# Optimization experiments

Measured on AMD Instinct MI355X. Metric: run time of the kernel, lower is better.

Reference implementation:

```python
import jax, jax.numpy as jnp
import numpy as np

# mamba-130m dims (n_layers reduced to 4 for single-device tractability)
B, L, D, DI, N, R, K, V, NL = 2, 512, 768, 1536, 16, 48, 4, 50280, 4


def setup_inputs() -> dict:
    key = jax.random.key(0)
    ks = jax.random.split(key, 10)
    s = 0.02
    return {
        "question_ids": jax.random.randint(ks[0], (B, L), 0, V, dtype=jnp.int32),
        "question_mask": jnp.ones((B, L), dtype=jnp.int32),
        "answer_ids": jax.random.randint(ks[1], (B, L), 0, V, dtype=jnp.int32),
        "answer_mask": jnp.ones((B, L), dtype=jnp.int32),
        "embed": jax.random.normal(ks[2], (V, D), jnp.float32) * s,
        "in_proj_w": jax.random.normal(ks[3], (NL, D, 2 * DI), jnp.float32) * s,
        "conv_w": jax.random.normal(ks[4], (NL, DI, K), jnp.float32) * s,
        "conv_b": jnp.zeros((NL, DI), jnp.float32),
        "x_proj_w": jax.random.normal(ks[5], (NL, DI, R + 2 * N), jnp.float32) * s,
        "dt_proj_w": jax.random.normal(ks[6], (NL, R, DI), jnp.float32) * s,
        # bias ~ -4.6 so softplus(dt) ~ 0.01, like mamba's dt init range
        "dt_proj_b": jnp.full((NL, DI), -4.6, jnp.float32),
        "A_log": jnp.broadcast_to(jnp.log(jnp.arange(1, N + 1, dtype=jnp.float32)), (NL, DI, N)) + jnp.zeros((NL, DI, N), jnp.float32),
        "D_param": jnp.ones((NL, DI), jnp.float32),
        "out_proj_w": jax.random.normal(ks[7], (NL, DI, D), jnp.float32) * s,
        "norm_w": jnp.ones((NL, D), jnp.float32),
        "norm_f_w": jnp.ones((D,), jnp.float32),
    }


def _rms(x, w, eps=1e-5):
    return x * jax.lax.rsqrt(jnp.mean(x * x, axis=-1, keepdims=True) + eps) * w


def _selective_scan(dA, dBu, Ct):
    # dA, dBu: (B, L, DI, N); Ct: (B, L, N)
    def step(h, xs):
        a, b = xs
        h = a * h + b
        return h, h

    h0 = jnp.zeros((dA.shape[0], dA.shape[2], dA.shape[3]), dA.dtype)  # (B, DI, N)
    _, hs = jax.lax.scan(step, h0, (jnp.swapaxes(dA, 0, 1), jnp.swapaxes(dBu, 0, 1)))
    hs = jnp.swapaxes(hs, 0, 1)  # (B, L, DI, N)
    return jnp.einsum('bldn,bln->bld', hs, Ct)


def _block(x, p):
    ipw, cw, cb, xpw, dtw, dtb, Alog, Dp, opw, nw = p
    h = _rms(x, nw)
    xz = h @ ipw                      # (B, L, 2*DI)
    u, z = xz[..., :DI], xz[..., DI:]
    # depthwise causal conv, kernel K
    up = jnp.pad(u, ((0, 0), (K - 1, 0), (0, 0)))
    uc = sum(up[:, k:k + u.shape[1], :] * cw[:, k] for k in range(K)) + cb
    uc = jax.nn.silu(uc)
    proj = uc @ xpw                   # (B, L, R+2N)
    dt = jax.nn.softplus(proj[..., :R] @ dtw + dtb)
    Bt = proj[..., R:R + N]
    Ct = proj[..., R + N:]
    A = -jnp.exp(Alog)                # (DI, N)
    dA = jnp.exp(dt[..., None] * A)   # (B, L, DI, N)
    dBu = (dt * uc)[..., None] * Bt[:, :, None, :]
    y = _selective_scan(dA, dBu, Ct) + uc * Dp
    y = y * jax.nn.silu(z)
    return x + y @ opw


def _lm_loss(ids, mask, embed, layers, norm_f_w):
    x = embed[ids] * mask[..., None].astype(embed.dtype)
    for p in layers:
        x = _block(x, p)
    x = _rms(x, norm_f_w)
    logits = x @ embed.T              # tied lm head, (B, L, V)
    logp = jax.nn.log_softmax(logits[:, :-1], axis=-1)
    lbl = ids[:, 1:]
    nll = -jnp.take_along_axis(logp, lbl[..., None], axis=-1)[..., 0]
    m = mask[:, 1:].astype(logp.dtype)
    return jnp.sum(nll * m) / jnp.maximum(jnp.sum(m), 1.0)


def reference(question_ids, question_mask, answer_ids, answer_mask, embed, in_proj_w, conv_w, conv_b, x_proj_w, dt_proj_w, dt_proj_b, A_log, D_param, out_proj_w, norm_w, norm_f_w):
    layers = [
        (in_proj_w[l], conv_w[l], conv_b[l], x_proj_w[l], dt_proj_w[l], dt_proj_b[l], A_log[l], D_param[l], out_proj_w[l], norm_w[l])
        for l in range(NL)
    ]
    loss_q = _lm_loss(question_ids, question_mask, embed, layers, norm_f_w)
    loss_a = _lm_loss(answer_ids, answer_mask, embed, layers, norm_f_w)
    return loss_a + loss_q
```

## Files before the change

### kernel.cpp

```cpp
#include <hip/hip_runtime.h>
#include <hip/hip_bf16.h>
#include <cstdint>
#include <cstddef>

#define T_TOK   2048
#define DM      768
#define DI      1536
#define NST     16
#define RRANK   48
#define KCONV   4
#define VOCAB   50280
#define NLAYER  4
#define SEQL    512
#define NTILE_V 197
#define NCHUNK  8
#define CHL     64
#define NCAT    1568

typedef __bf16 bf16x8 __attribute__((ext_vector_type(8)));
typedef float  f32x4  __attribute__((ext_vector_type(4)));

__device__ inline unsigned short f2b(float f) {
  union { float f; unsigned u; } v; v.f = f;
  unsigned r = v.u + 0x7FFFu + ((v.u >> 16) & 1u);
  return (unsigned short)(r >> 16);
}
__device__ inline float b2f(unsigned short h) {
  union { unsigned u; float f; } v; v.u = ((unsigned)h) << 16;
  return v.f;
}

__device__ inline void gload_lds16(const unsigned short* g, unsigned short* l) {
  __builtin_amdgcn_global_load_lds(
      (const __attribute__((address_space(1))) void*)g,
      (__attribute__((address_space(3))) void*)l, 16, 0, 0);
}

__global__ __launch_bounds__(256) void transpose_conv_kernel(
    const float* __restrict__ src, unsigned short* __restrict__ dst,
    int R, int C, int Rpad) {
  __shared__ float tile[32][33];
  const float* s = src + (size_t)blockIdx.z * R * C;
  unsigned short* d = dst + (size_t)blockIdx.z * C * Rpad;
  int c0 = blockIdx.x * 32, r0 = blockIdx.y * 32;
  int tx = threadIdx.x & 31, ty = threadIdx.x >> 5;
  #pragma unroll
  for (int i = 0; i < 32; i += 8) {
    int r = r0 + ty + i, c = c0 + tx;
    tile[ty + i][tx] = (r < R && c < C) ? s[(size_t)r * C + c] : 0.f;
  }
  __syncthreads();
  #pragma unroll
  for (int i = 0; i < 32; i += 8) {
    int c = c0 + ty + i, r = r0 + tx;
    if (c < C && r < Rpad) d[(size_t)c * Rpad + r] = f2b(tile[tx][ty + i]);
  }
}

__global__ __launch_bounds__(256) void cvt_embed_kernel(
    const float* __restrict__ e, unsigned short* __restrict__ eb) {
  const int n4 = VOCAB * DM / 4;
  for (int i = blockIdx.x * 256 + threadIdx.x; i < n4; i += gridDim.x * 256) {
    float4 f = *(const float4*)(e + (size_t)i * 4);
    union { unsigned long long u; unsigned short h[4]; } pk;
    pk.h[0] = f2b(f.x); pk.h[1] = f2b(f.y); pk.h[2] = f2b(f.z); pk.h[3] = f2b(f.w);
    *(unsigned long long*)(eb + (size_t)i * 4) = pk.u;
  }
}

__global__ __launch_bounds__(256) void wcat_bc_kernel(
    const float* __restrict__ xpw, unsigned short* __restrict__ wcat) {
  int l = blockIdx.y;
  int idx = blockIdx.x * 256 + threadIdx.x;
  int n = idx / DI, k = idx - n * DI;
  wcat[(size_t)l * NCAT * DI + (size_t)n * DI + k] =
      f2b(xpw[(size_t)l * DI * 80 + (size_t)k * 80 + 48 + n]);
}

__global__ __launch_bounds__(256) void wdt_kernel(
    const float* __restrict__ xpw, const float* __restrict__ dtw,
    unsigned short* __restrict__ wcat) {
  __shared__ float xs[64][49];
  __shared__ float ds[48][64];
  int l = blockIdx.z;
  int k0 = blockIdx.x * 64, n0 = blockIdx.y * 64;
  const float* xp = xpw + (size_t)l * DI * 80;
  const float* dp = dtw + (size_t)l * RRANK * DI;
  int tid = threadIdx.x;
  {
    int row = tid >> 2, cg = (tid & 3) * 12;
    #pragma unroll
    for (int c = 0; c < 12; ++c)
      xs[row][cg + c] = xp[(size_t)(k0 + row) * 80 + cg + c];
    int col = tid & 63, rb = tid >> 6;
    #pragma unroll
    for (int i = 0; i < 12; ++i)
      ds[rb + 4 * i][col] = dp[(size_t)(rb + 4 * i) * DI + n0 + col];
  }
  __syncthreads();
  int tx = tid & 63, ty = tid >> 6;
  float acc[16] = {};
  #pragma unroll 8
  for (int r = 0; r < 48; ++r) {
    float xv = xs[tx][r];
    #pragma unroll
    for (int i = 0; i < 16; ++i) acc[i] += xv * ds[r][ty + 4 * i];
  }
  unsigned short* wl = wcat + (size_t)l * NCAT * DI + (size_t)(32 + n0) * DI;
  #pragma unroll
  for (int i = 0; i < 16; ++i)
    wl[(size_t)(ty + 4 * i) * DI + k0 + tx] = f2b(acc[i]);
}

__global__ __launch_bounds__(256) void gather_rms_kernel(
    const int* __restrict__ qids, const int* __restrict__ qmask,
    const int* __restrict__ aids, const int* __restrict__ amask,
    const float* __restrict__ embed, const float* __restrict__ w,
    float* __restrict__ x, unsigned short* __restrict__ h) {
  int t = blockIdx.x;
  int seq = t >> 9, pos = t & 511;
  const int* ids = (seq < 2) ? qids : aids;
  const int* msk = (seq < 2) ? qmask : amask;
  int s2 = seq & 1;
  int id = ids[s2 * SEQL + pos];
  float m = (float)msk[s2 * SEQL + pos];
  const float* er = embed + (size_t)id * DM;
  float v[3], ss = 0.f;
  #pragma unroll
  for (int j = 0; j < 3; ++j) {
    int d = threadIdx.x + j * 256;
    float vv = er[d] * m;
    x[(size_t)t * DM + d] = vv;
    v[j] = vv; ss += vv * vv;
  }
  for (int o = 1; o < 64; o <<= 1) ss += __shfl_xor(ss, o);
  __shared__ float wsum[4];
  if ((threadIdx.x & 63) == 0) wsum[threadIdx.x >> 6] = ss;
  __syncthreads();
  ss = wsum[0] + wsum[1] + wsum[2] + wsum[3];
  float sc = rsqrtf(ss / (float)DM + 1e-5f);
  #pragma unroll
  for (int j = 0; j < 3; ++j) {
    int d = threadIdx.x + j * 256;
    h[(size_t)t * DM + d] = f2b(v[j] * sc * w[d]);
  }
}

__global__ __launch_bounds__(256) void resid_rms_kernel(
    float* __restrict__ x, const float* __restrict__ part,
    const float* __restrict__ w, unsigned short* __restrict__ h) {
  int t = blockIdx.x;
  float v[3];
  float ss = 0.f;
  #pragma unroll
  for (int j = 0; j < 3; ++j) {
    int d = threadIdx.x + j * 256;
    size_t o = (size_t)t * DM + d;
    float xv = x[o] + part[o] + part[(size_t)T_TOK * DM + o] +
               part[(size_t)2 * T_TOK * DM + o] + part[(size_t)3 * T_TOK * DM + o];
    x[o] = xv; v[j] = xv; ss += xv * xv;
  }
  for (int o = 1; o < 64; o <<= 1) ss += __shfl_xor(ss, o);
  __shared__ float wsum[4];
  if ((threadIdx.x & 63) == 0) wsum[threadIdx.x >> 6] = ss;
  __syncthreads();
  ss = wsum[0] + wsum[1] + wsum[2] + wsum[3];
  float sc = rsqrtf(ss / (float)DM + 1e-5f);
  #pragma unroll
  for (int j = 0; j < 3; ++j) {
    int d = threadIdx.x + j * 256;
    h[(size_t)t * DM + d] = f2b(v[j] * sc * w[d]);
  }
}

template <int EPI>
__global__ __launch_bounds__(256) void gemm_bf16_kernel(
    const unsigned short* __restrict__ A, int lda,
    const unsigned short* __restrict__ B, int ldb,
    float* __restrict__ C, float* __restrict__ CT, int ldc,
    const float* __restrict__ bias,
    int M, int N, int K, int mtiles) {
  __shared__ __attribute__((aligned(16))) unsigned short As[128 * 64];
  __shared__ __attribute__((aligned(16))) unsigned short Bs[128 * 64];
  int bid = blockIdx.x;
  int m0 = (bid % mtiles) * 128;
  int rest = bid / mtiles;
  int n0, split = 0;
  int ntil = (N + 127) >> 7;
  if (EPI == 6) { split = rest / ntil; n0 = (rest % ntil) * 128; }
  else n0 = rest * 128;
  const unsigned short* Ap = (EPI == 6) ? A + (size_t)split * K : A;
  const unsigned short* Bp = (EPI == 6) ? B + (size_t)split * K : B;
  int tid = threadIdx.x;
  int lane = tid & 63, w = tid >> 6;
  int wr = w >> 1, wc = w & 1;
  f32x4 acc[4][4] = {};

  int lrow = lane >> 3;
  int lcol = (((lane & 7) ^ (lrow & 7)) & 7) * 8;
  auto STAGE = [&](int k0) {
    #pragma unroll
    for (int it = 0; it < 4; ++it) {
      int r = w * 32 + it * 8;
      gload_lds16(Ap + (size_t)(m0 + r + lrow) * lda + k0 + lcol, &As[r * 64]);
      int br = n0 + r + lrow; if (br > N - 1) br = N - 1;
      gload_lds16(Bp + (size_t)br * ldb + k0 + lcol, &Bs[r * 64]);
    }
  };

  int nst = K / 64;
  int rA = wr * 64 + (lane & 15);
  int rB = wc * 64 + (lane & 15);
  int sw = lane & 7, ckb = lane >> 4;
  for (int s = 0; s < nst; ++s) {
    STAGE(s * 64);
    __syncthreads();
    __builtin_amdgcn_s_setprio(1);
    #pragma unroll
    for (int ks = 0; ks < 2; ++ks) {
      int ca = (((ks * 4 + ckb) ^ sw) & 7) * 8;
      bf16x8 a[4], b[4];
      #pragma unroll
      for (int i = 0; i < 4; ++i) a[i] = *(const bf16x8*)(&As[(rA + i * 16) * 64 + ca]);
      #pragma unroll
      for (int i = 0; i < 4; ++i) b[i] = *(const bf16x8*)(&Bs[(rB + i * 16) * 64 + ca]);
      #pragma unroll
      for (int mi = 0; mi < 4; ++mi)
        #pragma unroll
        for (int ni = 0; ni < 4; ++ni)
          acc[mi][ni] = __builtin_amdgcn_mfma_f32_16x16x32_bf16(a[mi], b[ni], acc[mi][ni], 0, 0, 0);
    }
    __builtin_amdgcn_s_setprio(0);
    __syncthreads();
  }

  int g = lane >> 4, c = lane & 15;
  #pragma unroll
  for (int mi = 0; mi < 4; ++mi)
    #pragma unroll
    for (int ni = 0; ni < 4; ++ni) {
      int col = n0 + wc * 64 + ni * 16 + c;
      int row0 = m0 + wr * 64 + mi * 16 + g * 4;
      if (EPI == 6) {
        if (col < N) {
          #pragma unroll
          for (int r = 0; r < 4; ++r)
            C[((size_t)split * M + row0 + r) * ldc + col] = acc[mi][ni][r];
        }
      }
      if (EPI == 7) {
        if (col < DI) {
          #pragma unroll
          for (int r = 0; r < 4; ++r)
            C[(size_t)(row0 + r) * DI + col] = acc[mi][ni][r];
        } else {
          float4 o; float* ov = (float*)&o;
          #pragma unroll
          for (int r = 0; r < 4; ++r) {
            float zv = acc[mi][ni][r];
            ov[r] = zv / (1.f + __expf(-zv));
          }
          *(float4*)(&CT[(size_t)(col - DI) * T_TOK + row0]) = o;
        }
      }
      if (EPI == 8) {
        if (col < 32) {
          float4 o; float* ov = (float*)&o;
          #pragma unroll
          for (int r = 0; r < 4; ++r) ov[r] = acc[mi][ni][r];
          *(float4*)(&C[(size_t)col * T_TOK + row0]) = o;
        } else if (col < NCAT) {
          float4 o; float* ov = (float*)&o;
          #pragma unroll
          for (int r = 0; r < 4; ++r) {
            float xv = acc[mi][ni][r] + bias[col - 32];
            ov[r] = (xv > 20.f) ? xv : log1pf(__expf(xv));
          }
          *(float4*)(&CT[(size_t)(col - 32) * T_TOK + row0]) = o;
        }
      }
    }
}

__global__ __launch_bounds__(512) void gemm_lse_kernel(
    const unsigned short* __restrict__ A,
    const unsigned short* __restrict__ B,
    float* __restrict__ pmax, float* __restrict__ psum,
    int mtiles) {
  __shared__ __attribute__((aligned(16))) unsigned short As[128 * 64];
  __shared__ __attribute__((aligned(16))) unsigned short Bs[256 * 64];
  __shared__ float lmax[128][4];
  __shared__ float lsum[128][4];
  const int K = DM, Nv = VOCAB;
  int bid = blockIdx.x;
  int m0 = (bid % mtiles) * 128;
  int n0 = (bid / mtiles) * 256;
  int tid = threadIdx.x;
  int lane = tid & 63, w = tid >> 6;
  int wr = w >> 2, wc = w & 3;
  f32x4 acc[4][4] = {};

  int lrow = lane >> 3;
  int lcol = (((lane & 7) ^ (lrow & 7)) & 7) * 8;
  auto STAGE = [&](int k0) {
    #pragma unroll
    for (int it = 0; it < 2; ++it) {
      int r = w * 16 + it * 8;
      gload_lds16(A + (size_t)(m0 + r + lrow) * K + k0 + lcol, &As[r * 64]);
    }
    #pragma unroll
    for (int it = 0; it < 4; ++it) {
      int r = w * 32 + it * 8;
      int br = n0 + r + lrow; if (br > Nv - 1) br = Nv - 1;
      gload_lds16(B + (size_t)br * K + k0 + lcol, &Bs[r * 64]);
    }
  };

  const int nst = K / 64;
  int rA = wr * 64 + (lane & 15);
  int rB = wc * 64 + (lane & 15);
  int sw = lane & 7, ckb = lane >> 4;
  for (int s = 0; s < nst; ++s) {
    STAGE(s * 64);
    __syncthreads();
    __builtin_amdgcn_s_setprio(1);
    #pragma unroll
    for (int ks = 0; ks < 2; ++ks) {
      int ca = (((ks * 4 + ckb) ^ sw) & 7) * 8;
      bf16x8 a[4], b[4];
      #pragma unroll
      for (int i = 0; i < 4; ++i) a[i] = *(const bf16x8*)(&As[(rA + i * 16) * 64 + ca]);
      #pragma unroll
      for (int i = 0; i < 4; ++i) b[i] = *(const bf16x8*)(&Bs[(rB + i * 16) * 64 + ca]);
      #pragma unroll
      for (int mi = 0; mi < 4; ++mi)
        #pragma unroll
        for (int ni = 0; ni < 4; ++ni)
          acc[mi][ni] = __builtin_amdgcn_mfma_f32_16x16x32_bf16(a[mi], b[ni], acc[mi][ni], 0, 0, 0);
    }
    __builtin_amdgcn_s_setprio(0);
    __syncthreads();
  }

  int g = lane >> 4, c = lane & 15;
  #pragma unroll
  for (int mi = 0; mi < 4; ++mi) {
    #pragma unroll
    for (int r = 0; r < 4; ++r) {
      float mx = -INFINITY;
      #pragma unroll
      for (int ni = 0; ni < 4; ++ni) {
        int col = n0 + wc * 64 + ni * 16 + c;
        float v = (col < Nv) ? acc[mi][ni][r] : -INFINITY;
        mx = fmaxf(mx, v);
      }
      mx = fmaxf(mx, __shfl_xor(mx, 1, 16));
      mx = fmaxf(mx, __shfl_xor(mx, 2, 16));
      mx = fmaxf(mx, __shfl_xor(mx, 4, 16));
      mx = fmaxf(mx, __shfl_xor(mx, 8, 16));
      float ssum = 0.f;
      #pragma unroll
      for (int ni = 0; ni < 4; ++ni) {
        int col = n0 + wc * 64 + ni * 16 + c;
        if (col < Nv) ssum += __expf(acc[mi][ni][r] - mx);
      }
      ssum += __shfl_xor(ssum, 1, 16);
      ssum += __shfl_xor(ssum, 2, 16);
      ssum += __shfl_xor(ssum, 4, 16);
      ssum += __shfl_xor(ssum, 8, 16);
      if (c == 0) {
        int rl = wr * 64 + mi * 16 + g * 4 + r;
        lmax[rl][wc] = mx;
        lsum[rl][wc] = ssum;
      }
    }
  }
  __syncthreads();
  if (tid < 128) {
    float m0v = lmax[tid][0], m1 = lmax[tid][1], m2 = lmax[tid][2], m3 = lmax[tid][3];
    float Mx = fmaxf(fmaxf(m0v, m1), fmaxf(m2, m3));
    float S = lsum[tid][0] * __expf(m0v - Mx) + lsum[tid][1] * __expf(m1 - Mx) +
              lsum[tid][2] * __expf(m2 - Mx) + lsum[tid][3] * __expf(m3 - Mx);
    int row = m0 + tid;
    int nb = n0 >> 8;
    pmax[(size_t)row * NTILE_V + nb] = Mx;
    psum[(size_t)row * NTILE_V + nb] = S;
  }
}

__global__ __launch_bounds__(256) void conv_silu_kernel(
    const float* __restrict__ ur, const float* __restrict__ cw,
    const float* __restrict__ cb,
    unsigned short* __restrict__ ucbf, float* __restrict__ ucT) {
  __shared__ float xu[67][64];
  __shared__ float ou[64][65];
  int t0 = blockIdx.x * 64;
  int ch0 = blockIdx.y * 64;
  int tid = threadIdx.x;
  int cx = tid & 63, ty = tid >> 6;
  bool seq_start = (t0 & 511) == 0;
  for (int r = ty; r < 67; r += 4) {
    int tg = t0 - 3 + r;
    float v = 0.f;
    if (r >= 3 || !seq_start) v = ur[(size_t)tg * DI + ch0 + cx];
    xu[r][cx] = v;
  }
  __syncthreads();
  int ch = ch0 + cx;
  float4 wv = *(const float4*)(cw + ch * 4);
  float bias = cb[ch];
  #pragma unroll
  for (int i = 0; i < 16; ++i) {
    int tr = ty * 16 + i;
    float a = bias + xu[tr][cx] * wv.x + xu[tr + 1][cx] * wv.y +
              xu[tr + 2][cx] * wv.z + xu[tr + 3][cx] * wv.w;
    float s = a / (1.f + __expf(-a));
    ucbf[(size_t)(t0 + tr) * DI + ch] = f2b(s);
    ou[tr][cx] = s;
  }
  __syncthreads();
  int tx = tid & 63, cy = tid >> 6;
  #pragma unroll
  for (int i = 0; i < 16; ++i) {
    int chi = cy * 16 + i;
    ucT[(size_t)(ch0 + chi) * T_TOK + t0 + tx] = ou[tx][chi];
  }
}

__global__ __launch_bounds__(256) void scan_sum_kernel(
    const float* __restrict__ dtT, const float* __restrict__ ucT,
    const float* __restrict__ BCt, const float* __restrict__ Alog,
    float* __restrict__ Pbuf, float* __restrict__ Fbuf) {
  int bc = blockIdx.x / 96;
  int idx = (blockIdx.x % 96) * 256 + threadIdx.x;
  int n = idx & 15, d = idx >> 4;
  int b = bc >> 3, chunk = bc & 7;
  float A = -__expf(Alog[d * NST + n]);
  int t0 = b * SEQL + chunk * CHL;
  const float4* dp = (const float4*)(dtT + (size_t)d * T_TOK + t0);
  const float4* up = (const float4*)(ucT + (size_t)d * T_TOK + t0);
  const float4* Bp = (const float4*)(BCt + (size_t)n * T_TOK + t0);
  float h = 0.f, sdt = 0.f;
  #pragma unroll
  for (int q = 0; q < CHL / 4; ++q) {
    float4 d4 = dp[q], u4 = up[q], B4 = Bp[q];
    float a;
    a = __expf(d4.x * A); h = fmaf(a, h, d4.x * u4.x * B4.x);
    a = __expf(d4.y * A); h = fmaf(a, h, d4.y * u4.y * B4.y);
    a = __expf(d4.z * A); h = fmaf(a, h, d4.z * u4.z * B4.z);
    a = __expf(d4.w * A); h = fmaf(a, h, d4.w * u4.w * B4.w);
    sdt += d4.x + d4.y + d4.z + d4.w;
  }
  size_t s = ((size_t)bc * DI + d) * NST + n;
  Pbuf[s] = __expf(A * sdt);
  Fbuf[s] = h;
}

__global__ __launch_bounds__(256) void scan_emit_kernel(
    const float* __restrict__ dtT, const float* __restrict__ ucT,
    const float* __restrict__ BCt, const float* __restrict__ zsT,
    const float* __restrict__ Alog, const float* __restrict__ Dpar,
    const float* __restrict__ Pbuf, const float* __restrict__ Fbuf,
    unsigned short* __restrict__ yg) {
  int bc = blockIdx.x / 96;
  int idx = (blockIdx.x % 96) * 256 + threadIdx.x;
  int n = idx & 15, d = idx >> 4;
  int b = bc >> 3, chunk = bc & 7;
  float A = -__expf(Alog[d * NST + n]);
  float Dpv = Dpar[d];
  float h = 0.f;
  for (int j = 0; j < chunk; ++j) {
    size_t s = (((size_t)(b * NCHUNK + j)) * DI + d) * NST + n;
    h = Fbuf[s] + Pbuf[s] * h;
  }
  int t0 = b * SEQL + chunk * CHL;
  const float4* dp = (const float4*)(dtT + (size_t)d * T_TOK + t0);
  const float4* up = (const float4*)(ucT + (size_t)d * T_TOK + t0);
  const float4* Bp = (const float4*)(BCt + (size_t)n * T_TOK + t0);
  const float4* Cp = (const float4*)(BCt + (size_t)(NST + n) * T_TOK + t0);
  const float4* zp = (const float4*)(zsT + (size_t)d * T_TOK + t0);
  unsigned short* yp = yg + (size_t)t0 * DI + d;
  #pragma unroll 4
  for (int q = 0; q < CHL / 4; ++q) {
    float4 d4 = dp[q], u4 = up[q], B4 = Bp[q], C4 = Cp[q], z4 = zp[q];
    float y0, y1, y2, y3, a, cc;
    a = __expf(d4.x * A); h = fmaf(a, h, d4.x * u4.x * B4.x); cc = h * C4.x;
    cc += __shfl_xor(cc, 1, 16); cc += __shfl_xor(cc, 2, 16);
    cc += __shfl_xor(cc, 4, 16); cc += __shfl_xor(cc, 8, 16);
    y0 = (cc + u4.x * Dpv) * z4.x;
    a = __expf(d4.y * A); h = fmaf(a, h, d4.y * u4.y * B4.y); cc = h * C4.y;
    cc += __shfl_xor(cc, 1, 16); cc += __shfl_xor(cc, 2, 16);
    cc += __shfl_xor(cc, 4, 16); cc += __shfl_xor(cc, 8, 16);
    y1 = (cc + u4.y * Dpv) * z4.y;
    a = __expf(d4.z * A); h = fmaf(a, h, d4.z * u4.z * B4.z); cc = h * C4.z;
    cc += __shfl_xor(cc, 1, 16); cc += __shfl_xor(cc, 2, 16);
    cc += __shfl_xor(cc, 4, 16); cc += __shfl_xor(cc, 8, 16);
    y2 = (cc + u4.z * Dpv) * z4.z;
    a = __expf(d4.w * A); h = fmaf(a, h, d4.w * u4.w * B4.w); cc = h * C4.w;
    cc += __shfl_xor(cc, 1, 16); cc += __shfl_xor(cc, 2, 16);
    cc += __shfl_xor(cc, 4, 16); cc += __shfl_xor(cc, 8, 16);
    y3 = (cc + u4.w * Dpv) * z4.w;
    if (n == 0) {
      yp[(size_t)(q * 4 + 0) * DI] = f2b(y0);
      yp[(size_t)(q * 4 + 1) * DI] = f2b(y1);
      yp[(size_t)(q * 4 + 2) * DI] = f2b(y2);
      yp[(size_t)(q * 4 + 3) * DI] = f2b(y3);
    }
  }
}

__global__ __launch_bounds__(256) void lse_label_kernel(
    const float* __restrict__ pmax, const float* __restrict__ psum,
    const unsigned short* __restrict__ h, const unsigned short* __restrict__ eb,
    const int* __restrict__ qids, const int* __restrict__ qmask,
    const int* __restrict__ aids, const int* __restrict__ amask,
    float* __restrict__ nllm, float* __restrict__ mrow) {
  int row = blockIdx.x * 4 + (threadIdx.x >> 6);
  int lane = threadIdx.x & 63;
  const float* pm = pmax + (size_t)row * NTILE_V;
  const float* ps = psum + (size_t)row * NTILE_V;
  float m = -INFINITY;
  for (int j = lane; j < NTILE_V; j += 64) m = fmaxf(m, pm[j]);
  for (int o = 1; o < 64; o <<= 1) m = fmaxf(m, __shfl_xor(m, o));
  float s = 0.f;
  for (int j = lane; j < NTILE_V; j += 64) s += ps[j] * __expf(pm[j] - m);
  for (int o = 1; o < 64; o <<= 1) s += __shfl_xor(s, o);
  float lse = m + __logf(s);
  int pos = row & 511, seq = row >> 9;
  float nll = 0.f, mv = 0.f;
  if (pos != 511) {
    const int* ids = (seq < 2) ? qids : aids;
    const int* msk = (seq < 2) ? qmask : amask;
    int lbl = ids[(seq & 1) * SEQL + pos + 1];
    mv = (float)msk[(seq & 1) * SEQL + pos + 1];
    const unsigned short* hr = h + (size_t)row * DM;
    const unsigned short* er = eb + (size_t)lbl * DM;
    float dt = 0.f;
    for (int k = lane; k < DM; k += 64) dt += b2f(hr[k]) * b2f(er[k]);
    for (int o = 1; o < 64; o <<= 1) dt += __shfl_xor(dt, o);
    nll = (lse - dt) * mv;
  }
  if (lane == 0) { nllm[row] = nll; mrow[row] = mv; }
}

__global__ __launch_bounds__(256) void loss2_kernel(
    const float* __restrict__ nllm, const float* __restrict__ mrow,
    float* __restrict__ out) {
  float nq = 0.f, dq = 0.f, na = 0.f, da = 0.f;
  for (int row = threadIdx.x; row < T_TOK; row += 256) {
    int seq = row >> 9;
    if (seq < 2) { nq += nllm[row]; dq += mrow[row]; }
    else         { na += nllm[row]; da += mrow[row]; }
  }
  for (int o = 1; o < 64; o <<= 1) {
    nq += __shfl_xor(nq, o); dq += __shfl_xor(dq, o);
    na += __shfl_xor(na, o); da += __shfl_xor(da, o);
  }
  __shared__ float red[4][4];
  int w = threadIdx.x >> 6;
  if ((threadIdx.x & 63) == 0) { red[w][0] = nq; red[w][1] = dq; red[w][2] = na; red[w][3] = da; }
  __syncthreads();
  if (threadIdx.x == 0) {
    nq = 0.f; dq = 0.f; na = 0.f; da = 0.f;
    for (int i = 0; i < 4; ++i) { nq += red[i][0]; dq += red[i][1]; na += red[i][2]; da += red[i][3]; }
    float lq = nq / fmaxf(dq, 1.f);
    float la = na / fmaxf(da, 1.f);
    out[0] = lq + la;
  }
}

extern "C" void kernel_launch(void* const* d_in, const int* in_sizes, int n_in,
                              void* d_out, int out_size, void* d_ws, size_t ws_size,
                              hipStream_t stream) {
  const int*   qids  = (const int*)d_in[0];
  const int*   qmask = (const int*)d_in[1];
  const int*   aids  = (const int*)d_in[2];
  const int*   amask = (const int*)d_in[3];
  const float* embed = (const float*)d_in[4];
  const float* ipw   = (const float*)d_in[5];
  const float* cw    = (const float*)d_in[6];
  const float* cb    = (const float*)d_in[7];
  const float* xpw   = (const float*)d_in[8];
  const float* dtw   = (const float*)d_in[9];
  const float* dtb   = (const float*)d_in[10];
  const float* Alog  = (const float*)d_in[11];
  const float* Dp    = (const float*)d_in[12];
  const float* opw   = (const float*)d_in[13];
  const float* nw    = (const float*)d_in[14];
  const float* nfw   = (const float*)d_in[15];

  char* wp = (char*)d_ws;
  auto alloc = [&](size_t bytes) { char* p = wp; wp += (bytes + 255) & ~(size_t)255; return p; };

  float*          x      = (float*)alloc((size_t)T_TOK * DM * 4);
  unsigned short* hbf    = (unsigned short*)alloc((size_t)T_TOK * DM * 2);
  float*          ur     = (float*)alloc((size_t)T_TOK * DI * 4);
  unsigned short* ucbf   = (unsigned short*)alloc((size_t)T_TOK * DI * 2);
  unsigned short* ygbf   = (unsigned short*)alloc((size_t)T_TOK * DI * 2);
  float*          ucT    = (float*)alloc((size_t)DI * T_TOK * 4);
  float*          zsT    = (float*)alloc((size_t)DI * T_TOK * 4);
  float*          dtT    = (float*)alloc((size_t)DI * T_TOK * 4);
  float*          BCt    = (float*)alloc((size_t)2 * NST * T_TOK * 4);
  float*          Pbuf   = (float*)alloc((size_t)4 * NCHUNK * DI * NST * 4);
  float*          Fbuf   = (float*)alloc((size_t)4 * NCHUNK * DI * NST * 4);
  float*          opart  = (float*)alloc((size_t)4 * T_TOK * DM * 4);
  unsigned short* ipw_t  = (unsigned short*)alloc((size_t)NLAYER * 2 * DI * DM * 2);
  unsigned short* opw_t  = (unsigned short*)alloc((size_t)NLAYER * DM * DI * 2);
  unsigned short* wcat   = (unsigned short*)alloc((size_t)NLAYER * NCAT * DI * 2);
  unsigned short* embbf  = (unsigned short*)alloc((size_t)VOCAB * DM * 2);
  float*          pmax   = (float*)alloc((size_t)T_TOK * NTILE_V * 4);
  float*          psum   = (float*)alloc((size_t)T_TOK * NTILE_V * 4);
  float*          nllm   = (float*)alloc((size_t)T_TOK * 4);
  float*          mrow   = (float*)alloc((size_t)T_TOK * 4);

  transpose_conv_kernel<<<dim3(96, 24, NLAYER), 256, 0, stream>>>(ipw, ipw_t, DM, 2 * DI, DM);
  transpose_conv_kernel<<<dim3(24, 48, NLAYER), 256, 0, stream>>>(opw, opw_t, DI, DM, DI);
  cvt_embed_kernel<<<2048, 256, 0, stream>>>(embed, embbf);
  wcat_bc_kernel<<<dim3(192, NLAYER), 256, 0, stream>>>(xpw, wcat);
  wdt_kernel<<<dim3(24, 24, NLAYER), 256, 0, stream>>>(xpw, dtw, wcat);

  gather_rms_kernel<<<T_TOK, 256, 0, stream>>>(qids, qmask, aids, amask, embed, nw, x, hbf);

  const int mt = T_TOK / 128;
  for (int l = 0; l < NLAYER; ++l) {
    gemm_bf16_kernel<7><<<mt * (2 * DI / 128), 256, 0, stream>>>(
        hbf, DM, ipw_t + (size_t)l * 2 * DI * DM, DM, ur, zsT, DI,
        nullptr, T_TOK, 2 * DI, DM, mt);
    conv_silu_kernel<<<dim3(T_TOK / 64, DI / 64), 256, 0, stream>>>(
        ur, cw + (size_t)l * DI * KCONV, cb + (size_t)l * DI, ucbf, ucT);
    gemm_bf16_kernel<8><<<mt * 13, 256, 0, stream>>>(
        ucbf, DI, wcat + (size_t)l * NCAT * DI, DI, BCt, dtT, 0,
        dtb + (size_t)l * DI, T_TOK, NCAT, DI, mt);
    scan_sum_kernel<<<32 * 96, 256, 0, stream>>>(
        dtT, ucT, BCt, Alog + (size_t)l * DI * NST, Pbuf, Fbuf);
    scan_emit_kernel<<<32 * 96, 256, 0, stream>>>(
        dtT, ucT, BCt, zsT, Alog + (size_t)l * DI * NST, Dp + (size_t)l * DI,
        Pbuf, Fbuf, ygbf);
    gemm_bf16_kernel<6><<<mt * (DM / 128) * 4, 256, 0, stream>>>(
        ygbf, DI, opw_t + (size_t)l * DM * DI, DI, opart, nullptr, DM,
        nullptr, T_TOK, DM, DI / 4, mt);
    resid_rms_kernel<<<T_TOK, 256, 0, stream>>>(
        x, opart, (l < NLAYER - 1) ? (nw + (l + 1) * DM) : nfw, hbf);
  }

  gemm_lse_kernel<<<mt * NTILE_V, 512, 0, stream>>>(hbf, embbf, pmax, psum, mt);
  lse_label_kernel<<<T_TOK / 4, 256, 0, stream>>>(
      pmax, psum, hbf, embbf, qids, qmask, aids, amask, nllm, mrow);
  loss2_kernel<<<1, 256, 0, stream>>>(nllm, mrow, (float*)d_out);
}
```

Measured before the change: 1.181 ms.

## Unfold fused x_proj/dt_proj weight into low-rank two-GEMM chain

Previously the dt part of x_proj was pre-multiplied with dt_proj into a 1568-wide concatenated weight, making each layer's projection a full 2048x1568x1536 GEMM. Now x_proj runs as a narrow 80-column split-K GEMM, followed by a reduce kernel that writes the bf16 projection and the B/C rows. A separate K=64 GEMM with a softplus epilogue then produces dt. This exploits the rank-48 bottleneck to cut FLOPs sharply, at the cost of two extra launches and a partial-sum round trip per layer.

```diff
diff --git a/kernel.cpp b/kernel.cpp
--- a/kernel.cpp
+++ b/kernel.cpp
@@ -15,7 +15,6 @@
 #define NTILE_V 197
 #define NCHUNK  8
 #define CHL     64
-#define NCAT    1568
 
 typedef __bf16 bf16x8 __attribute__((ext_vector_type(8)));
 typedef float  f32x4  __attribute__((ext_vector_type(4)));
@@ -66,50 +65,6 @@
     pk.h[0] = f2b(f.x); pk.h[1] = f2b(f.y); pk.h[2] = f2b(f.z); pk.h[3] = f2b(f.w);
     *(unsigned long long*)(eb + (size_t)i * 4) = pk.u;
   }
-}
-
-__global__ __launch_bounds__(256) void wcat_bc_kernel(
-    const float* __restrict__ xpw, unsigned short* __restrict__ wcat) {
-  int l = blockIdx.y;
-  int idx = blockIdx.x * 256 + threadIdx.x;
-  int n = idx / DI, k = idx - n * DI;
-  wcat[(size_t)l * NCAT * DI + (size_t)n * DI + k] =
-      f2b(xpw[(size_t)l * DI * 80 + (size_t)k * 80 + 48 + n]);
-}
-
-__global__ __launch_bounds__(256) void wdt_kernel(
-    const float* __restrict__ xpw, const float* __restrict__ dtw,
-    unsigned short* __restrict__ wcat) {
-  __shared__ float xs[64][49];
-  __shared__ float ds[48][64];
-  int l = blockIdx.z;
-  int k0 = blockIdx.x * 64, n0 = blockIdx.y * 64;
-  const float* xp = xpw + (size_t)l * DI * 80;
-  const float* dp = dtw + (size_t)l * RRANK * DI;
-  int tid = threadIdx.x;
-  {
-    int row = tid >> 2, cg = (tid & 3) * 12;
-    #pragma unroll
-    for (int c = 0; c < 12; ++c)
-      xs[row][cg + c] = xp[(size_t)(k0 + row) * 80 + cg + c];
-    int col = tid & 63, rb = tid >> 6;
-    #pragma unroll
-    for (int i = 0; i < 12; ++i)
-      ds[rb + 4 * i][col] = dp[(size_t)(rb + 4 * i) * DI + n0 + col];
-  }
-  __syncthreads();
-  int tx = tid & 63, ty = tid >> 6;
-  float acc[16] = {};
-  #pragma unroll 8
-  for (int r = 0; r < 48; ++r) {
-    float xv = xs[tx][r];
-    #pragma unroll
-    for (int i = 0; i < 16; ++i) acc[i] += xv * ds[r][ty + 4 * i];
-  }
-  unsigned short* wl = wcat + (size_t)l * NCAT * DI + (size_t)(32 + n0) * DI;
-  #pragma unroll
-  for (int i = 0; i < 16; ++i)
-    wl[(size_t)(ty + 4 * i) * DI + k0 + tx] = f2b(acc[i]);
 }
 
 __global__ __launch_bounds__(256) void gather_rms_kernel(
@@ -241,6 +196,17 @@
     for (int ni = 0; ni < 4; ++ni) {
       int col = n0 + wc * 64 + ni * 16 + c;
       int row0 = m0 + wr * 64 + mi * 16 + g * 4;
+      if (EPI == 5) {
+        if (col < N) {
+          float4 o; float* ov = (float*)&o;
+          #pragma unroll
+          for (int r = 0; r < 4; ++r) {
+            float xv = acc[mi][ni][r] + bias[col];
+            ov[r] = (xv > 20.f) ? xv : log1pf(__expf(xv));
+          }
+          *(float4*)(&CT[(size_t)col * T_TOK + row0]) = o;
+        }
+      }
       if (EPI == 6) {
         if (col < N) {
           #pragma unroll
@@ -263,23 +229,18 @@
           *(float4*)(&CT[(size_t)(col - DI) * T_TOK + row0]) = o;
         }
       }
-      if (EPI == 8) {
-        if (col < 32) {
-          float4 o; float* ov = (float*)&o;
-          #pragma unroll
-          for (int r = 0; r < 4; ++r) ov[r] = acc[mi][ni][r];
-          *(float4*)(&C[(size_t)col * T_TOK + row0]) = o;
-        } else if (col < NCAT) {
-          float4 o; float* ov = (float*)&o;
-          #pragma unroll
-          for (int r = 0; r < 4; ++r) {
-            float xv = acc[mi][ni][r] + bias[col - 32];
-            ov[r] = (xv > 20.f) ? xv : log1pf(__expf(xv));
-          }
-          *(float4*)(&CT[(size_t)(col - 32) * T_TOK + row0]) = o;
-        }
-      }
-    }
+    }
+}
+
+__global__ __launch_bounds__(256) void xproj_reduce_kernel(
+    const float* __restrict__ part, unsigned short* __restrict__ projbf,
+    float* __restrict__ BCt) {
+  int idx = blockIdx.x * 256 + threadIdx.x;
+  int row = idx / 80, col = idx - row * 80;
+  float v = part[idx] + part[(size_t)T_TOK * 80 + idx] +
+            part[(size_t)2 * T_TOK * 80 + idx] + part[(size_t)3 * T_TOK * 80 + idx];
+  projbf[idx] = f2b(v);
+  if (col >= RRANK) BCt[(size_t)(col - RRANK) * T_TOK + row] = v;
 }
 
 __global__ __launch_bounds__(512) void gemm_lse_kernel(
@@ -596,6 +557,7 @@
   unsigned short* hbf    = (unsigned short*)alloc((size_t)T_TOK * DM * 2);
   float*          ur     = (float*)alloc((size_t)T_TOK * DI * 4);
   unsigned short* ucbf   = (unsigned short*)alloc((size_t)T_TOK * DI * 2);
+  unsigned short* projbf = (unsigned short*)alloc((size_t)T_TOK * 80 * 2);
   unsigned short* ygbf   = (unsigned short*)alloc((size_t)T_TOK * DI * 2);
   float*          ucT    = (float*)alloc((size_t)DI * T_TOK * 4);
   float*          zsT    = (float*)alloc((size_t)DI * T_TOK * 4);
@@ -603,10 +565,12 @@
   float*          BCt    = (float*)alloc((size_t)2 * NST * T_TOK * 4);
   float*          Pbuf   = (float*)alloc((size_t)4 * NCHUNK * DI * NST * 4);
   float*          Fbuf   = (float*)alloc((size_t)4 * NCHUNK * DI * NST * 4);
+  float*          xpart  = (float*)alloc((size_t)4 * T_TOK * 80 * 4);
   float*          opart  = (float*)alloc((size_t)4 * T_TOK * DM * 4);
   unsigned short* ipw_t  = (unsigned short*)alloc((size_t)NLAYER * 2 * DI * DM * 2);
   unsigned short* opw_t  = (unsigned short*)alloc((size_t)NLAYER * DM * DI * 2);
-  unsigned short* wcat   = (unsigned short*)alloc((size_t)NLAYER * NCAT * DI * 2);
+  unsigned short* xpw_t  = (unsigned short*)alloc((size_t)NLAYER * 80 * DI * 2);
+  unsigned short* dtw_t  = (unsigned short*)alloc((size_t)NLAYER * DI * 64 * 2);
   unsigned short* embbf  = (unsigned short*)alloc((size_t)VOCAB * DM * 2);
   float*          pmax   = (float*)alloc((size_t)T_TOK * NTILE_V * 4);
   float*          psum   = (float*)alloc((size_t)T_TOK * NTILE_V * 4);
@@ -615,9 +579,9 @@
 
   transpose_conv_kernel<<<dim3(96, 24, NLAYER), 256, 0, stream>>>(ipw, ipw_t, DM, 2 * DI, DM);
   transpose_conv_kernel<<<dim3(24, 48, NLAYER), 256, 0, stream>>>(opw, opw_t, DI, DM, DI);
+  transpose_conv_kernel<<<dim3(3, 48, NLAYER), 256, 0, stream>>>(xpw, xpw_t, DI, 80, DI);
+  transpose_conv_kernel<<<dim3(48, 2, NLAYER), 256, 0, stream>>>(dtw, dtw_t, RRANK, DI, 64);
   cvt_embed_kernel<<<2048, 256, 0, stream>>>(embed, embbf);
-  wcat_bc_kernel<<<dim3(192, NLAYER), 256, 0, stream>>>(xpw, wcat);
-  wdt_kernel<<<dim3(24, 24, NLAYER), 256, 0, stream>>>(xpw, dtw, wcat);
 
   gather_rms_kernel<<<T_TOK, 256, 0, stream>>>(qids, qmask, aids, amask, embed, nw, x, hbf);
 
@@ -628,9 +592,13 @@
         nullptr, T_TOK, 2 * DI, DM, mt);
     conv_silu_kernel<<<dim3(T_TOK / 64, DI / 64), 256, 0, stream>>>(
         ur, cw + (size_t)l * DI * KCONV, cb + (size_t)l * DI, ucbf, ucT);
-    gemm_bf16_kernel<8><<<mt * 13, 256, 0, stream>>>(
-        ucbf, DI, wcat + (size_t)l * NCAT * DI, DI, BCt, dtT, 0,
-        dtb + (size_t)l * DI, T_TOK, NCAT, DI, mt);
+    gemm_bf16_kernel<6><<<mt * 1 * 4, 256, 0, stream>>>(
+        ucbf, DI, xpw_t + (size_t)l * 80 * DI, DI, xpart, nullptr, 80,
+        nullptr, T_TOK, 80, DI / 4, mt);
+    xproj_reduce_kernel<<<(T_TOK * 80) / 256, 256, 0, stream>>>(xpart, projbf, BCt);
+    gemm_bf16_kernel<5><<<mt * (DI / 128), 256, 0, stream>>>(
+        projbf, 80, dtw_t + (size_t)l * DI * 64, 64, nullptr, dtT, DI,
+        dtb + (size_t)l * DI, T_TOK, DI, 64, mt);
     scan_sum_kernel<<<32 * 96, 256, 0, stream>>>(
         dtT, ucT, BCt, Alog + (size_t)l * DI * NST, Pbuf, Fbuf);
     scan_emit_kernel<<<32 * 96, 256, 0, stream>>>(
```

Result: faster. 1.115 ms (-5.6%).
